# Kernel optimization log

Measured on AMD Instinct MI355X. Metric: run time of the kernel, lower is better.

## Reference

```python
import jax, jax.numpy as jnp
import numpy as np

B, S, D, H, NH, C = 32, 512, 768, 768, 4, 10
HD = H // NH


def _lin(x, w, b):
    return x @ w.T + b


def _ln(x, g, b, eps=1e-5):
    mu = jnp.mean(x, axis=-1, keepdims=True)
    var = jnp.mean(jnp.square(x - mu), axis=-1, keepdims=True)
    return (x - mu) * jax.lax.rsqrt(var + eps) * g + b


def setup_inputs() -> dict:
    key = jax.random.key(0)
    ks = jax.random.split(key, 16)
    w = lambda k, shape: jax.random.normal(k, shape, dtype=jnp.float32) * 0.02
    return {
        "x": jax.random.normal(ks[0], (B, S, D), dtype=jnp.float32),
        "wq": w(ks[1], (H, D)), "bq": jnp.zeros((H,), jnp.float32),
        "wk": w(ks[2], (H, D)), "bk": jnp.zeros((H,), jnp.float32),
        "wv": w(ks[3], (H, D)), "bv": jnp.zeros((H,), jnp.float32),
        "wx": w(ks[4], (H, D)), "bx": jnp.zeros((H,), jnp.float32),
        "in_proj_w": w(ks[5], (3 * H, H)), "in_proj_b": jnp.zeros((3 * H,), jnp.float32),
        "out_proj_w": w(ks[6], (H, H)), "out_proj_b": jnp.zeros((H,), jnp.float32),
        "fc1a_w": w(ks[7], (H, H)), "fc1a_b": jnp.zeros((H,), jnp.float32),
        "fc1b_w": w(ks[8], (H, H)), "fc1b_b": jnp.zeros((H,), jnp.float32),
        "ln_g": jnp.ones((H,), jnp.float32), "ln_b": jnp.zeros((H,), jnp.float32),
        "fc2_w": w(ks[9], (C, H)), "fc2_b": jnp.zeros((C,), jnp.float32),
    }


def reference(x, wq, bq, wk, bk, wv, bv, wx, bx, in_proj_w, in_proj_b,
              out_proj_w, out_proj_b, fc1a_w, fc1a_b, fc1b_w, fc1b_b,
              ln_g, ln_b, fc2_w, fc2_b):
    # Vectorized sinusoidal PE matching the triple loop:
    # even i: sin(pos / 10000^(2i/D)); odd i: cos(pos / 10000^(2(i-1)/D))
    d = x.shape[2]
    pos = jnp.arange(x.shape[1], dtype=x.dtype)[:, None]          # [S,1]
    i = jnp.arange(d)
    i_even = (i - (i % 2)).astype(x.dtype)                        # 2*(i - i%2)/d exponent
    angle = pos / jnp.power(jnp.asarray(10000.0, x.dtype), 2.0 * i_even / d)  # [S,D]
    pe = jnp.where(i % 2 == 0, jnp.sin(angle), jnp.cos(angle))
    x = x + pe[None]

    q = _lin(x, wq, bq)
    k = _lin(x, wk, bk)
    v = _lin(x, wv, bv)
    xr = _lin(x, wx, bx)

    # torch MultiheadAttention: in_proj, split heads, SDPA, out_proj
    wq_i, wk_i, wv_i = jnp.split(in_proj_w, 3, axis=0)
    bq_i, bk_i, bv_i = jnp.split(in_proj_b, 3, axis=0)
    b = x.shape[0]
    q2 = _lin(q, wq_i, bq_i).reshape(b, -1, NH, HD)
    k2 = _lin(k, wk_i, bk_i).reshape(b, -1, NH, HD)
    v2 = _lin(v, wv_i, bv_i).reshape(b, -1, NH, HD)
    scores = jnp.einsum('bqhd,bkhd->bhqk', q2, k2) / jnp.sqrt(jnp.asarray(HD, x.dtype))
    attn = jax.nn.softmax(scores, axis=-1)
    ctx = jnp.einsum('bhqk,bkhd->bqhd', attn, v2).reshape(b, -1, H)
    attn_out = _lin(ctx, out_proj_w, out_proj_b)

    x = _ln(xr + attn_out, ln_g, ln_b)
    ffn = _lin(jax.nn.relu(_lin(x, fc1a_w, fc1a_b)), fc1b_w, fc1b_b)
    x = _ln(x + ffn, ln_g, ln_b)
    x = jnp.sum(x, axis=1)
    return _lin(x, fc2_w, fc2_b)
```

## Files before the change

kernel.cpp:

```cpp
#include <hip/hip_runtime.h>
#include <hip/hip_bf16.h>

typedef __bf16 bf16;
typedef __bf16 bf16x8 __attribute__((ext_vector_type(8)));
typedef __bf16 bf16x4 __attribute__((ext_vector_type(4)));
typedef __bf16 bf16x2 __attribute__((ext_vector_type(2)));
typedef float  f32x4  __attribute__((ext_vector_type(4)));

#define GLD16(g, l) __builtin_amdgcn_global_load_lds(                        \
    (const __attribute__((address_space(1))) void*)(g),                      \
    (__attribute__((address_space(3))) void*)(l), 16, 0, 0)

template<int BM, int BN, int MFR, int NFR>
__global__ __launch_bounds__(256, 3)
void gemm_nt(const bf16* __restrict__ A, const bf16* __restrict__ B,
             bf16* __restrict__ C, const float* __restrict__ bias,
             int K, int lda, int ldb, int ldc,
             int inner,
             long long aOut, long long aIn,
             long long bOut, long long bIn,
             long long cOut, long long cIn,
             float alpha, int relu,
             const bf16* __restrict__ res, int ldr)
{
    const int z  = blockIdx.z;
    const int zo = z / inner;
    const int zi = z - zo * inner;
    A += (long long)zo * aOut + (long long)zi * aIn;
    B += (long long)zo * bOut + (long long)zi * bIn;
    C += (long long)zo * cOut + (long long)zi * cIn;

    const int tm = blockIdx.y * BM;
    const int tn = blockIdx.x * BN;

    __shared__ __align__(16) bf16 smem[(BM + BN) * 64];
    bf16* As = smem;
    bf16* Bs = smem + BM * 64;

    const int tid  = threadIdx.x;
    const int lane = tid & 63;
    const int wid  = tid >> 6;
    const int wr   = wid >> 1;
    const int wc   = wid & 1;

    f32x4 acc[MFR][NFR];
#pragma unroll
    for (int i = 0; i < MFR; ++i)
#pragma unroll
        for (int j = 0; j < NFR; ++j) acc[i][j] = (f32x4){0.f, 0.f, 0.f, 0.f};

    const int srow = lane >> 3;
    const int gch8 = ((lane & 7) ^ srow) * 8;

    const int NA = BM / 32;
    const int NB = BN / 32;

    const bf16* aP[NA];
#pragma unroll
    for (int jj = 0; jj < NA; ++jj) {
        const int R0 = (wid * NA + jj) * 8;
        aP[jj] = A + (long long)(tm + R0 + srow) * lda + gch8;
    }
    const bf16* bP[NB];
#pragma unroll
    for (int jj = 0; jj < NB; ++jj) {
        const int R0 = (wid * NB + jj) * 8;
        bP[jj] = B + (long long)(tn + R0 + srow) * ldb + gch8;
    }

    const int lr = lane & 15;
    const int qg = lane >> 4;

    for (int kt = 0; kt < K; kt += 64) {
#pragma unroll
        for (int jj = 0; jj < NA; ++jj)
            GLD16(aP[jj], As + (wid * NA + jj) * 512);
#pragma unroll
        for (int jj = 0; jj < NB; ++jj)
            GLD16(bP[jj], Bs + (wid * NB + jj) * 512);
        __syncthreads();

#pragma unroll
        for (int h = 0; h < 2; ++h) {
            const int off = ((qg + h * 4) ^ (lr & 7)) * 8;
            bf16x8 af[MFR], bfr[NFR];
#pragma unroll
            for (int i = 0; i < MFR; ++i)
                af[i] = *(const bf16x8*)(As + (wr * MFR * 16 + i * 16 + lr) * 64 + off);
#pragma unroll
            for (int j = 0; j < NFR; ++j)
                bfr[j] = *(const bf16x8*)(Bs + (wc * NFR * 16 + j * 16 + lr) * 64 + off);
#pragma unroll
            for (int i = 0; i < MFR; ++i)
#pragma unroll
                for (int j = 0; j < NFR; ++j)
                    acc[i][j] = __builtin_amdgcn_mfma_f32_16x16x32_bf16(
                        af[i], bfr[j], acc[i][j], 0, 0, 0);
        }
        __syncthreads();
#pragma unroll
        for (int jj = 0; jj < NA; ++jj) aP[jj] += 64;
#pragma unroll
        for (int jj = 0; jj < NB; ++jj) bP[jj] += 64;
    }

#pragma unroll
    for (int i = 0; i < MFR; ++i) {
#pragma unroll
        for (int j = 0; j < NFR; ++j) {
            const int mm0 = tm + wr * MFR * 16 + i * 16 + (lane >> 4) * 4;
            const int nn  = tn + wc * NFR * 16 + j * 16 + (lane & 15);
#pragma unroll
            for (int r = 0; r < 4; ++r) {
                float v = acc[i][j][r] * alpha;
                if (bias) v += bias[nn];
                if (res)  v += (float)res[(long long)(mm0 + r) * ldr + nn];
                if (relu) v = fmaxf(v, 0.f);
                C[(long long)(mm0 + r) * ldc + nn] = (bf16)v;
            }
        }
    }
}

#define BAR8()  __builtin_amdgcn_s_barrier()

#define RD_A(S, MB)                                                          \
    _Pragma("unroll") for (int mi = 0; mi < 4; ++mi)                         \
    _Pragma("unroll") for (int h = 0; h < 2; ++h)                            \
        af[mi][h] = *(const bf16x8*)((S) + aBase + ((MB) + mi) * 1024 +      \
                                     (h ? koff1 : koff0));

#define RD_B(S, NJ)                                                          \
    _Pragma("unroll") for (int h = 0; h < 2; ++h)                            \
        bfv[NJ][h] = *(const bf16x8*)((S) + bBase + (NJ) * 1024 +            \
                                      (h ? koff1 : koff0));

#define MFMA_Q(MB, N0, N1)                                                   \
    _Pragma("unroll") for (int h = 0; h < 2; ++h)                            \
    _Pragma("unroll") for (int mi = 0; mi < 4; ++mi) {                       \
        acc[(MB)+mi][(N0)] = __builtin_amdgcn_mfma_f32_16x16x32_bf16(        \
            af[mi][h], bfv[(N0)][h], acc[(MB)+mi][(N0)], 0, 0, 0);           \
        acc[(MB)+mi][(N1)] = __builtin_amdgcn_mfma_f32_16x16x32_bf16(        \
            af[mi][h], bfv[(N1)][h], acc[(MB)+mi][(N1)], 0, 0, 0);           \
    }

#define MFMA_Q1(MB, N0)                                                      \
    _Pragma("unroll") for (int h = 0; h < 2; ++h)                            \
    _Pragma("unroll") for (int mi = 0; mi < 4; ++mi) {                       \
        acc[(MB)+mi][(N0)] = __builtin_amdgcn_mfma_f32_16x16x32_bf16(        \
            af[mi][h], bfv[(N0)][h], acc[(MB)+mi][(N0)], 0, 0, 0);           \
    }

#define STAGE_A(DST)                                                         \
    _Pragma("unroll") for (int jj = 0; jj < 4; ++jj) {                       \
        GLD16(aP[jj], (DST) + (wid * 4 + jj) * 512);  aP[jj] += 64; }

#define STAGE_B(DST)                                                         \
    _Pragma("unroll") for (int jj = 0; jj < 4; ++jj) {                       \
        GLD16(bP[jj], (DST) + 16384 + (wid * 4 + jj) * 512);  bP[jj] += 64; }

#define STAGE_B3(DST)                                                        \
    _Pragma("unroll") for (int jj = 0; jj < 3; ++jj) {                       \
        GLD16(bP[jj], (DST) + 16384 + (wid * 3 + jj) * 512);  bP[jj] += 64; }

#define END_TILE()                                                           \
    asm volatile("s_waitcnt vmcnt(0)" ::: "memory");                         \
    __builtin_amdgcn_sched_barrier(0);                                       \
    BAR8();

#define K_TILE_F(CUR, NXT, STG, LAST)                                        \
  {                                                                          \
    RD_A((CUR), 0);                                                          \
    RD_B((CUR), 0); RD_B((CUR), 1); RD_B((CUR), 2); RD_B((CUR), 3);          \
    if (STG) { STAGE_A(NXT) STAGE_B(NXT) }                                   \
    MFMA_Q(0, 0, 1)                                                          \
    MFMA_Q(0, 2, 3)                                                          \
    RD_A((CUR), 4);                                                          \
    MFMA_Q(4, 2, 3)                                                          \
    MFMA_Q(4, 0, 1)                                                          \
    if (!(LAST)) { END_TILE() }                                              \
  }

#define K_TILE_F3(CUR, NXT, STG, LAST)                                       \
  {                                                                          \
    RD_A((CUR), 0);                                                          \
    RD_B((CUR), 0); RD_B((CUR), 1); RD_B((CUR), 2);                          \
    if (STG) { STAGE_A(NXT) STAGE_B3(NXT) }                                  \
    MFMA_Q(0, 0, 1)                                                          \
    MFMA_Q1(0, 2)                                                            \
    RD_A((CUR), 4);                                                          \
    MFMA_Q1(4, 2)                                                            \
    MFMA_Q(4, 0, 1)                                                          \
    if (!(LAST)) { END_TILE() }                                              \
  }

__global__ __launch_bounds__(512, 2)
void gemm_qkv_8ph(const bf16* __restrict__ A, const bf16* __restrict__ B,
                  bf16* __restrict__ C, const float* __restrict__ bias)
{
    constexpr int LDA = 768, LDB = 768, LDC = 3072;
    const int tm = blockIdx.y * 256;
    const int tn = blockIdx.x * 256;

    __shared__ __align__(16) bf16 smem[2][2 * 256 * 64];

    const int tid  = threadIdx.x;
    const int lane = tid & 63;
    const int wid  = tid >> 6;
    const int wr   = wid >> 2;
    const int wc   = wid & 3;
    const int lr   = lane & 15;
    const int qg   = lane >> 4;

    const int srow = lane >> 3;
    const int gch8 = ((lane & 7) ^ srow) * 8;
    const bf16* aP[4];
    const bf16* bP[4];
#pragma unroll
    for (int jj = 0; jj < 4; ++jj) {
        aP[jj] = A + (long long)(tm + wid * 32 + jj * 8 + srow) * LDA + gch8;
        bP[jj] = B + (long long)(tn + wid * 32 + jj * 8 + srow) * LDB + gch8;
    }

    f32x4 acc[8][4];
#pragma unroll
    for (int i = 0; i < 8; ++i)
#pragma unroll
        for (int j = 0; j < 4; ++j) acc[i][j] = (f32x4){0.f, 0.f, 0.f, 0.f};

    const int aBase = (wr * 128 + lr) * 64;
    const int bBase = 16384 + (wc * 64 + lr) * 64;
    const int koff0 = ((qg    ) ^ (lr & 7)) * 8;
    const int koff1 = ((qg + 4) ^ (lr & 7)) * 8;

    bf16x8 af[4][2];
    bf16x8 bfv[4][2];

    bf16* S0 = &smem[0][0];
    bf16* S1 = &smem[1][0];

    STAGE_A(S0)
    STAGE_B(S0)
    asm volatile("s_waitcnt vmcnt(0)" ::: "memory");
    __builtin_amdgcn_sched_barrier(0);
    BAR8();

#pragma unroll 1
    for (int it = 0; it < 5; ++it) {
        K_TILE_F(S0, S1, 1, 0)
        K_TILE_F(S1, S0, 1, 0)
    }
    K_TILE_F(S0, S1, 1, 0)
    K_TILE_F(S1, S0, 0, 1)

    float bv[4];
#pragma unroll
    for (int j = 0; j < 4; ++j) bv[j] = bias[tn + wc * 64 + j * 16 + lr];

#pragma unroll
    for (int i = 0; i < 8; ++i) {
        const int mm0 = tm + wr * 128 + i * 16 + qg * 4;
#pragma unroll
        for (int j = 0; j < 4; ++j) {
            const int nn = tn + wc * 64 + j * 16 + lr;
#pragma unroll
            for (int r = 0; r < 4; ++r)
                C[(long long)(mm0 + r) * LDC + nn] = (bf16)(acc[i][j][r] + bv[j]);
        }
    }
}

__global__ __launch_bounds__(512, 2)
void gemm_flow(const bf16* __restrict__ A, const bf16* __restrict__ B,
               bf16* __restrict__ C, const float* __restrict__ bias,
               int lda, int ldb, int ldc, int relu,
               const bf16* __restrict__ res, int ldr)
{
    const int tm = blockIdx.y * 256;
    const int tn = blockIdx.x * 192;

    __shared__ __align__(16) bf16 smem[2][(256 + 192) * 64];

    const int tid  = threadIdx.x;
    const int lane = tid & 63;
    const int wid  = tid >> 6;
    const int wr   = wid >> 2;
    const int wc   = wid & 3;
    const int lr   = lane & 15;
    const int qg   = lane >> 4;

    const int srow = lane >> 3;
    const int gch8 = ((lane & 7) ^ srow) * 8;
    const bf16* aP[4];
    const bf16* bP[3];
#pragma unroll
    for (int jj = 0; jj < 4; ++jj)
        aP[jj] = A + (long long)(tm + wid * 32 + jj * 8 + srow) * lda + gch8;
#pragma unroll
    for (int jj = 0; jj < 3; ++jj)
        bP[jj] = B + (long long)(tn + wid * 24 + jj * 8 + srow) * ldb + gch8;

    f32x4 acc[8][3];
#pragma unroll
    for (int i = 0; i < 8; ++i)
#pragma unroll
        for (int j = 0; j < 3; ++j) acc[i][j] = (f32x4){0.f, 0.f, 0.f, 0.f};

    const int aBase = (wr * 128 + lr) * 64;
    const int bBase = 16384 + (wc * 48 + lr) * 64;
    const int koff0 = ((qg    ) ^ (lr & 7)) * 8;
    const int koff1 = ((qg + 4) ^ (lr & 7)) * 8;

    bf16x8 af[4][2];
    bf16x8 bfv[3][2];

    bf16* S0 = &smem[0][0];
    bf16* S1 = &smem[1][0];

    STAGE_A(S0)
    STAGE_B3(S0)
    asm volatile("s_waitcnt vmcnt(0)" ::: "memory");
    __builtin_amdgcn_sched_barrier(0);
    BAR8();

#pragma unroll 1
    for (int it = 0; it < 5; ++it) {
        K_TILE_F3(S0, S1, 1, 0)
        K_TILE_F3(S1, S0, 1, 0)
    }
    K_TILE_F3(S0, S1, 1, 0)
    K_TILE_F3(S1, S0, 0, 1)

    float bv[3];
#pragma unroll
    for (int j = 0; j < 3; ++j) bv[j] = bias ? bias[tn + wc * 48 + j * 16 + lr] : 0.f;

#pragma unroll
    for (int i = 0; i < 8; ++i) {
        const int mm0 = tm + wr * 128 + i * 16 + qg * 4;
#pragma unroll
        for (int j = 0; j < 3; ++j) {
            const int nn = tn + wc * 48 + j * 16 + lr;
#pragma unroll
            for (int r = 0; r < 4; ++r) {
                float v = acc[i][j][r] + bv[j];
                if (res)  v += (float)res[(long long)(mm0 + r) * ldr + nn];
                if (relu) v = fmaxf(v, 0.f);
                C[(long long)(mm0 + r) * ldc + nn] = (bf16)v;
            }
        }
    }
}

__global__ __launch_bounds__(256, 2)
void fused_attn_kernel(bf16* __restrict__ qkvx)
{
    const int flat = blockIdx.x;
    const int qt = (flat >> 3) & 3;
    const int z  = (flat & 7) | ((flat >> 5) << 3);
    const int b  = z >> 2, h = z & 3;

    const bf16* Qg = qkvx + (long long)b * 512 * 3072 + h * 192;
    const bf16* Kg = Qg + 768;
    const bf16* Vg = Qg + 1536;

    __shared__ __align__(16) bf16 Ks[64 * 192];
    __shared__ __align__(16) bf16 VTs[192 * 64];
    __shared__ __align__(16) bf16 Pb[4 * 32 * 64];

    const int tid  = threadIdx.x;
    const int lane = tid & 63;
    const int wid  = tid >> 6;
    const int lr   = lane & 15;
    const int qg   = lane >> 4;
    const int m0   = qt * 128 + wid * 32;

    bf16x8 qf[2][6];
#pragma unroll
    for (int mt = 0; mt < 2; ++mt)
#pragma unroll
        for (int t = 0; t < 6; ++t)
            qf[mt][t] = *(const bf16x8*)(Qg + (long long)(m0 + mt * 16 + lr) * 3072
                                         + t * 32 + qg * 8);

    const bf16* kP[6];
#pragma unroll
    for (int i = 0; i < 6; ++i) {
        const int c = i * 256 + tid;
        const int krow = c / 24, kcc = c % 24;
        const int kgc  = (kcc & 24) | ((kcc & 7) ^ (krow & 7));
        kP[i] = Kg + (long long)krow * 3072 + kgc * 8;
    }
    const int vkp = tid & 31;
    const int vdc = tid >> 5;

    f32x4 acc[2][12];
#pragma unroll
    for (int mt = 0; mt < 2; ++mt)
#pragma unroll
        for (int dt = 0; dt < 12; ++dt) acc[mt][dt] = (f32x4){0.f, 0.f, 0.f, 0.f};
    float mrow[2][4], lrow[2][4];
#pragma unroll
    for (int mt = 0; mt < 2; ++mt)
#pragma unroll
        for (int r = 0; r < 4; ++r) { mrow[mt][r] = -3e38f; lrow[mt][r] = 0.f; }

    const float alpha = 0.0721687836f;

    for (int kt = 0; kt < 8; ++kt) {
#pragma unroll
        for (int i = 0; i < 6; ++i)
            GLD16(kP[i], Ks + (i * 256 + wid * 64) * 8);
#pragma unroll
        for (int i = 0; i < 3; ++i) {
            const int dc = vdc + i * 8;
            const bf16* p = Vg + (long long)(2 * vkp) * 3072 + dc * 8;
            const bf16x8 v0 = *(const bf16x8*)(p);
            const bf16x8 v1 = *(const bf16x8*)(p + 3072);
#pragma unroll
            for (int j = 0; j < 8; ++j) {
                const int d = dc * 8 + j;
                bf16x2 pk; pk[0] = v0[j]; pk[1] = v1[j];
                *(bf16x2*)(VTs + d * 64 + ((vkp >> 2) ^ (d & 7)) * 8
                           + 2 * (vkp & 3)) = pk;
            }
        }
        __syncthreads();

        f32x4 sf[2][4];
#pragma unroll
        for (int mt = 0; mt < 2; ++mt)
#pragma unroll
            for (int nt = 0; nt < 4; ++nt) sf[mt][nt] = (f32x4){0.f, 0.f, 0.f, 0.f};
#pragma unroll
        for (int nt = 0; nt < 4; ++nt) {
#pragma unroll
            for (int t = 0; t < 6; ++t) {
                const int ch = t * 4 + qg;
                const int ph = (ch & 24) | ((ch & 7) ^ (lr & 7));
                const bf16x8 kf = *(const bf16x8*)(Ks + (nt * 16 + lr) * 192 + ph * 8);
                sf[0][nt] = __builtin_amdgcn_mfma_f32_16x16x32_bf16(qf[0][t], kf, sf[0][nt], 0, 0, 0);
                sf[1][nt] = __builtin_amdgcn_mfma_f32_16x16x32_bf16(qf[1][t], kf, sf[1][nt], 0, 0, 0);
            }
        }

#pragma unroll
        for (int mt = 0; mt < 2; ++mt) {
            float mx[4], a[4], rs[4], p[4][4];
#pragma unroll
            for (int r = 0; r < 4; ++r) {
                float v0 = fmaxf(sf[mt][0][r], sf[mt][1][r]);
                float v1 = fmaxf(sf[mt][2][r], sf[mt][3][r]);
                mx[r] = fmaxf(v0, v1) * alpha;
            }
#pragma unroll
            for (int msk = 1; msk <= 8; msk <<= 1)
#pragma unroll
                for (int r = 0; r < 4; ++r) mx[r] = fmaxf(mx[r], __shfl_xor(mx[r], msk));
#pragma unroll
            for (int r = 0; r < 4; ++r) {
                const float mn = fmaxf(mrow[mt][r], mx[r]);
                a[r] = __expf(mrow[mt][r] - mn);
                mrow[mt][r] = mn;
                rs[r] = 0.f;
            }
#pragma unroll
            for (int nt = 0; nt < 4; ++nt)
#pragma unroll
                for (int r = 0; r < 4; ++r) {
                    p[nt][r] = __expf(sf[mt][nt][r] * alpha - mrow[mt][r]);
                    rs[r] += p[nt][r];
                }
#pragma unroll
            for (int msk = 1; msk <= 8; msk <<= 1)
#pragma unroll
                for (int r = 0; r < 4; ++r) rs[r] += __shfl_xor(rs[r], msk);
#pragma unroll
            for (int r = 0; r < 4; ++r) lrow[mt][r] = lrow[mt][r] * a[r] + rs[r];
#pragma unroll
            for (int dt = 0; dt < 12; ++dt)
#pragma unroll
                for (int r = 0; r < 4; ++r) acc[mt][dt][r] *= a[r];
#pragma unroll
            for (int nt = 0; nt < 4; ++nt)
#pragma unroll
                for (int r = 0; r < 4; ++r) {
                    const int row = mt * 16 + qg * 4 + r;
                    const int ph2 = (nt * 2 + (lr >> 3)) ^ (row & 7);
                    Pb[wid * 2048 + row * 64 + ph2 * 8 + (lr & 7)] = (bf16)p[nt][r];
                }
        }

        bf16x8 pf[2][2];
#pragma unroll
        for (int mt = 0; mt < 2; ++mt)
#pragma unroll
            for (int ks = 0; ks < 2; ++ks) {
                const int row = mt * 16 + lr;
                const int ph  = (ks * 4 + qg) ^ (lr & 7);
                pf[mt][ks] = *(const bf16x8*)(Pb + wid * 2048 + row * 64 + ph * 8);
            }
#pragma unroll
        for (int dt = 0; dt < 12; ++dt) {
#pragma unroll
            for (int ks = 0; ks < 2; ++ks) {
                const int ph = (ks * 4 + qg) ^ (lr & 7);
                const bf16x8 vf = *(const bf16x8*)(VTs + (dt * 16 + lr) * 64 + ph * 8);
                acc[0][dt] = __builtin_amdgcn_mfma_f32_16x16x32_bf16(pf[0][ks], vf, acc[0][dt], 0, 0, 0);
                acc[1][dt] = __builtin_amdgcn_mfma_f32_16x16x32_bf16(pf[1][ks], vf, acc[1][dt], 0, 0, 0);
            }
        }
        __syncthreads();
#pragma unroll
        for (int i = 0; i < 6; ++i) kP[i] += 64 * 3072;
        Vg += 64 * 3072;
    }

    bf16* Og = qkvx + (long long)b * 512 * 3072 + h * 192;
#pragma unroll
    for (int mt = 0; mt < 2; ++mt) {
        float inv[4];
#pragma unroll
        for (int r = 0; r < 4; ++r) inv[r] = 1.0f / lrow[mt][r];
#pragma unroll
        for (int dt = 0; dt < 12; ++dt)
#pragma unroll
            for (int r = 0; r < 4; ++r) {
                const int row = m0 + mt * 16 + qg * 4 + r;
                Og[(long long)row * 3072 + dt * 16 + lr] = (bf16)(acc[mt][dt][r] * inv[r]);
            }
    }
}

__device__ __forceinline__ void cast4(const float* src, bf16* dst, int i)
{
    const float4 v = *(const float4*)(src + (long long)i * 4);
    bf16x4 o;
    o[0] = (bf16)v.x; o[1] = (bf16)v.y; o[2] = (bf16)v.z; o[3] = (bf16)v.w;
    *(bf16x4*)(dst + (long long)i * 4) = o;
}

__global__ __launch_bounds__(256)
void prep_kernel(const float* __restrict__ wq, const float* __restrict__ wk,
                 const float* __restrict__ wv, const float* __restrict__ wx,
                 const float* __restrict__ inpw, const float* __restrict__ inpb,
                 const float* __restrict__ bq, const float* __restrict__ bk,
                 const float* __restrict__ bv, const float* __restrict__ bx,
                 const float* __restrict__ woutp, const float* __restrict__ wf1a,
                 const float* __restrict__ wf1b, const float* __restrict__ x,
                 bf16* __restrict__ WT3, bf16* __restrict__ INPJ,
                 bf16* __restrict__ WOUT, bf16* __restrict__ WF1A,
                 bf16* __restrict__ WF1B, bf16* __restrict__ WXD,
                 float* __restrict__ BCAT, bf16* __restrict__ XPE)
{
    const int blk = blockIdx.x;
    const int tid = threadIdx.x;
    __shared__ bf16 t[32][33];

    if (blk < 1728) {
        const int which = blk / 576, local = blk - which * 576;
        const float* src = (which == 0) ? wq : ((which == 1) ? wk : wv);
        bf16* dst = WT3 + (long long)which * 589824;
        const int r0 = (local / 24) * 32, c0 = (local % 24) * 32;
        const int tr = tid >> 5, tc = tid & 31;
#pragma unroll
        for (int k = 0; k < 4; ++k) {
            const int r = tr + k * 8;
            t[r][tc] = (bf16)src[(long long)(r0 + r) * 768 + c0 + tc];
        }
        __syncthreads();
#pragma unroll
        for (int k = 0; k < 4; ++k) {
            const int c = tr + k * 8;
            dst[(long long)(c0 + c) * 768 + r0 + tc] = t[tc][c];
        }
    } else if (blk < 3456) {
        cast4(inpw, INPJ, (blk - 1728) * 256 + tid);
    } else if (blk < 4032) {
        cast4(woutp, WOUT, (blk - 3456) * 256 + tid);
    } else if (blk < 4608) {
        cast4(wf1a, WF1A, (blk - 4032) * 256 + tid);
    } else if (blk < 5184) {
        cast4(wf1b, WF1B, (blk - 4608) * 256 + tid);
    } else if (blk < 5760) {
        cast4(wx, WXD, (blk - 5184) * 256 + tid);
    } else if (blk < 6051) {
        const int bl = blk - 5760;
        if (bl < 288) {
            const int g = tid >> 5, l = tid & 31;
            const int n = bl * 8 + g;
            const int zsec = n / 768;
            const float* bb = (zsec == 0) ? bq : ((zsec == 1) ? bk : bv);
            const float* wrow = inpw + (long long)n * 768;
            float s = 0.f;
            for (int d = l; d < 768; d += 32) s += wrow[d] * bb[d];
#pragma unroll
            for (int off = 16; off; off >>= 1) s += __shfl_xor(s, off);
            if (l == 0) BCAT[n] = inpb[n] + s;
        } else {
            const int n = (bl - 288) * 256 + tid;
            if (n < 768) BCAT[2304 + n] = bx[n];
        }
    } else {
        const int idx4 = ((blk - 6051) * 256 + tid) * 4;
        const int d    = idx4 % 768;
        const int row  = idx4 / 768;
        const int s    = row & 511;
        const float ksc = -0.034603417655076f;
        const float4 xv = *(const float4*)(x + (long long)idx4);
        float a0 = (float)s * exp2f((float)d * ksc);
        float a1 = (float)s * exp2f((float)(d + 2) * ksc);
        float s0, c0, s1, c1;
        sincosf(a0, &s0, &c0);
        sincosf(a1, &s1, &c1);
        bf16x4 o;
        o[0] = (bf16)(xv.x + s0);
        o[1] = (bf16)(xv.y + c0);
        o[2] = (bf16)(xv.z + s1);
        o[3] = (bf16)(xv.w + c1);
        *(bf16x4*)(XPE + (long long)idx4) = o;
    }
}

__global__ __launch_bounds__(256)
void ln1_kernel(const bf16* __restrict__ a, int lda_,
                bf16* __restrict__ o, int ldo,
                const float* __restrict__ g, const float* __restrict__ be)
{
    const int blk  = blockIdx.x;
    const int tid  = threadIdx.x;
    const int wid  = tid >> 6, lane = tid & 63;
    const int d0   = lane * 12;

    float gv[12], ev[12];
#pragma unroll
    for (int k = 0; k < 12; k += 4) {
        *(float4*)(gv + k) = *(const float4*)(g + d0 + k);
        *(float4*)(ev + k) = *(const float4*)(be + d0 + k);
    }

    for (int i = 0; i < 8; ++i) {
        const int row = blk * 32 + i * 4 + wid;
        const bf16* p = a + (long long)row * lda_ + d0;
        float xv[12];
#pragma unroll
        for (int k = 0; k < 12; k += 4) {
            const bf16x4 v = *(const bf16x4*)(p + k);
            xv[k] = (float)v[0]; xv[k+1] = (float)v[1];
            xv[k+2] = (float)v[2]; xv[k+3] = (float)v[3];
        }
        float s1 = 0.f, s2 = 0.f;
#pragma unroll
        for (int k = 0; k < 12; ++k) { s1 += xv[k]; s2 += xv[k] * xv[k]; }
        for (int off = 32; off; off >>= 1) {
            s1 += __shfl_xor(s1, off);
            s2 += __shfl_xor(s2, off);
        }
        const float mu  = s1 * (1.0f / 768.0f);
        const float var = s2 * (1.0f / 768.0f) - mu * mu;
        const float rs  = rsqrtf(var + 1e-5f);
        bf16* po = o + (long long)row * ldo + d0;
#pragma unroll
        for (int k = 0; k < 12; k += 4) {
            bf16x4 ov;
            ov[0] = (bf16)((xv[k]   - mu) * rs * gv[k]   + ev[k]);
            ov[1] = (bf16)((xv[k+1] - mu) * rs * gv[k+1] + ev[k+1]);
            ov[2] = (bf16)((xv[k+2] - mu) * rs * gv[k+2] + ev[k+2]);
            ov[3] = (bf16)((xv[k+3] - mu) * rs * gv[k+3] + ev[k+3]);
            *(bf16x4*)(po + k) = ov;
        }
    }
}

__global__ __launch_bounds__(256)
void ln2_reduce_kernel(const bf16* __restrict__ src,
                       const float* __restrict__ g, const float* __restrict__ be,
                       float* __restrict__ partial)
{
    const int blk  = blockIdx.x;
    const int tid  = threadIdx.x;
    const int wid  = tid >> 6, lane = tid & 63;
    const int d0   = lane * 12;

    float gv[12], ev[12];
#pragma unroll
    for (int k = 0; k < 12; k += 4) {
        *(float4*)(gv + k) = *(const float4*)(g + d0 + k);
        *(float4*)(ev + k) = *(const float4*)(be + d0 + k);
    }
    float acc[12];
#pragma unroll
    for (int k = 0; k < 12; ++k) acc[k] = 0.f;

    for (int i = 0; i < 8; ++i) {
        const int row = blk * 32 + i * 4 + wid;
        const bf16* p = src + (long long)row * 3072 + d0;
        float xv[12];
#pragma unroll
        for (int k = 0; k < 12; k += 4) {
            const bf16x4 v = *(const bf16x4*)(p + k);
            xv[k] = (float)v[0]; xv[k+1] = (float)v[1];
            xv[k+2] = (float)v[2]; xv[k+3] = (float)v[3];
        }
        float s1 = 0.f, s2 = 0.f;
#pragma unroll
        for (int k = 0; k < 12; ++k) { s1 += xv[k]; s2 += xv[k] * xv[k]; }
        for (int off = 32; off; off >>= 1) {
            s1 += __shfl_xor(s1, off);
            s2 += __shfl_xor(s2, off);
        }
        const float mu  = s1 * (1.0f / 768.0f);
        const float var = s2 * (1.0f / 768.0f) - mu * mu;
        const float rs  = rsqrtf(var + 1e-5f);
#pragma unroll
        for (int k = 0; k < 12; ++k) acc[k] += (xv[k] - mu) * rs * gv[k] + ev[k];
    }

    __shared__ float red[4][768];
#pragma unroll
    for (int k = 0; k < 12; k += 4)
        *(float4*)(&red[wid][d0 + k]) = *(const float4*)(acc + k);
    __syncthreads();
    if (wid == 0) {
#pragma unroll
        for (int k = 0; k < 12; k += 4) {
            const float4 a0 = *(const float4*)(&red[0][d0 + k]);
            const float4 a1 = *(const float4*)(&red[1][d0 + k]);
            const float4 a2 = *(const float4*)(&red[2][d0 + k]);
            const float4 a3 = *(const float4*)(&red[3][d0 + k]);
            *(float4*)(partial + (long long)blk * 768 + d0 + k) =
                make_float4(a0.x + a1.x + a2.x + a3.x, a0.y + a1.y + a2.y + a3.y,
                            a0.z + a1.z + a2.z + a3.z, a0.w + a1.w + a2.w + a3.w);
        }
    }
}

__global__ __launch_bounds__(192)
void reduce_fc2_stage2_kernel(const float* __restrict__ partial, const float* __restrict__ w,
                              const float* __restrict__ bias, float* __restrict__ out)
{
    const int b = blockIdx.x, t = threadIdx.x;
    const int d0 = t * 4;
    float a[4] = {0.f, 0.f, 0.f, 0.f};
    for (int c = 0; c < 16; ++c) {
        const float4 pv = *(const float4*)(partial + (long long)(b * 16 + c) * 768 + d0);
        a[0] += pv.x; a[1] += pv.y; a[2] += pv.z; a[3] += pv.w;
    }
    __shared__ float os[10];
    if (t < 10) os[t] = 0.f;
    __syncthreads();
    for (int c = 0; c < 10; ++c) {
        const float4 wv = *(const float4*)(w + c * 768 + d0);
        float p = wv.x * a[0] + wv.y * a[1] + wv.z * a[2] + wv.w * a[3];
        for (int off = 32; off; off >>= 1) p += __shfl_xor(p, off);
        if ((t & 63) == 0) atomicAdd(&os[c], p);
    }
    __syncthreads();
    if (t < 10) out[b * 10 + t] = os[t] + bias[t];
}

static const size_t OFF_XPE  = 0;
static const size_t OFF_WCAT = OFF_XPE  + (size_t)16384 * 768 * 2;
static const size_t OFF_WT3  = OFF_WCAT + (size_t)3072 * 768 * 2;
static const size_t OFF_INPJ = OFF_WT3  + (size_t)3 * 768 * 768 * 2;
static const size_t OFF_WOUT = OFF_INPJ + (size_t)2304 * 768 * 2;
static const size_t OFF_WF1A = OFF_WOUT + (size_t)768 * 768 * 2;
static const size_t OFF_WF1B = OFF_WF1A + (size_t)768 * 768 * 2;
static const size_t OFF_BCAT = OFF_WF1B + (size_t)768 * 768 * 2;
static const size_t OFF_QKVX = OFF_BCAT + (size_t)3072 * 4;
static const size_t OFF_VT   = OFF_QKVX + (size_t)16384 * 3072 * 2;
static const size_t OFF_S    = OFF_VT   + (size_t)128 * 192 * 512 * 2;
static const size_t OFF_X1   = OFF_S    + (size_t)128 * 512 * 512 * 2;

extern "C" void kernel_launch(void* const* d_in, const int* in_sizes, int n_in,
                              void* d_out, int out_size, void* d_ws, size_t ws_size,
                              hipStream_t stream)
{
    const float* x     = (const float*)d_in[0];
    const float* wq    = (const float*)d_in[1];
    const float* bq    = (const float*)d_in[2];
    const float* wk    = (const float*)d_in[3];
    const float* bk    = (const float*)d_in[4];
    const float* wv    = (const float*)d_in[5];
    const float* bv    = (const float*)d_in[6];
    const float* wx    = (const float*)d_in[7];
    const float* bx    = (const float*)d_in[8];
    const float* inpw  = (const float*)d_in[9];
    const float* inpb  = (const float*)d_in[10];
    const float* woutp = (const float*)d_in[11];
    const float* boutp = (const float*)d_in[12];
    const float* wf1a  = (const float*)d_in[13];
    const float* bf1a  = (const float*)d_in[14];
    const float* wf1b  = (const float*)d_in[15];
    const float* bf1b  = (const float*)d_in[16];
    const float* lng   = (const float*)d_in[17];
    const float* lnb   = (const float*)d_in[18];
    const float* wfc2  = (const float*)d_in[19];
    const float* bfc2  = (const float*)d_in[20];
    float* out = (float*)d_out;

    char* ws = (char*)d_ws;
    bf16*  XPE  = (bf16*)(ws + OFF_XPE);
    bf16*  WCAT = (bf16*)(ws + OFF_WCAT);
    bf16*  WT3  = (bf16*)(ws + OFF_WT3);
    bf16*  INPJ = (bf16*)(ws + OFF_INPJ);
    bf16*  WOUT = (bf16*)(ws + OFF_WOUT);
    bf16*  WF1A = (bf16*)(ws + OFF_WF1A);
    bf16*  WF1B = (bf16*)(ws + OFF_WF1B);
    float* BCAT = (float*)(ws + OFF_BCAT);
    bf16*  QKVX = (bf16*)(ws + OFF_QKVX);
    float* PART = (float*)(ws + OFF_S);
    bf16*  X1   = (bf16*)(ws + OFF_X1);

    prep_kernel<<<18339, 256, 0, stream>>>(wq, wk, wv, wx, inpw, inpb,
                                           bq, bk, bv, bx, woutp, wf1a, wf1b, x,
                                           WT3, INPJ, WOUT, WF1A, WF1B,
                                           WCAT + (size_t)2304 * 768, BCAT, XPE);

    gemm_nt<64, 128, 2, 4><<<dim3(6, 12, 3), 256, 0, stream>>>(
        INPJ, WT3, WCAT, nullptr, 768, 768, 768, 768,
        1, 589824, 0, 589824, 0, 589824, 0, 1.0f, 0, nullptr, 0);

    gemm_qkv_8ph<<<dim3(12, 64, 1), 512, 0, stream>>>(XPE, WCAT, QKVX, BCAT);

    fused_attn_kernel<<<512, 256, 0, stream>>>(QKVX);

    gemm_flow<<<dim3(4, 64, 1), 512, 0, stream>>>(
        QKVX, WOUT, QKVX + 768, boutp, 3072, 768, 3072,
        0, QKVX + 2304, 3072);

    ln1_kernel<<<512, 256, 0, stream>>>(QKVX + 768, 3072, X1, 768, lng, lnb);

    gemm_flow<<<dim3(4, 64, 1), 512, 0, stream>>>(
        X1, WF1A, QKVX + 1536, bf1a, 768, 768, 3072,
        1, nullptr, 0);

    gemm_flow<<<dim3(4, 64, 1), 512, 0, stream>>>(
        QKVX + 1536, WF1B, QKVX + 2304, bf1b, 3072, 768, 3072,
        0, X1, 768);

    ln2_reduce_kernel<<<512, 256, 0, stream>>>(QKVX + 2304, lng, lnb, PART);

    reduce_fc2_stage2_kernel<<<32, 192, 0, stream>>>(PART, wfc2, bfc2, out);
}
```

Before: 443.7 us.

## Restructure QKV GEMM K-loop into phased in-place staging with wave priority

The QKV projection GEMM's main loop now preloads two K tiles and refills each shared-memory buffer in place as soon as its sub-tiles have been read, instead of staging the next tile at the start. Loads are interleaved between four MFMA phases separated by workgroup barriers, and the wait is relaxed to vmcnt(4) so one tile's loads stay in flight. MFMA phases run under raised wave priority via s_setprio. The aim is to overlap global-to-LDS traffic with compute and drop the full vmcnt(0) stall each tile, at the cost of extra barriers per tile and tighter correctness dependencies on barrier placement.

```diff
diff --git a/kernel.cpp b/kernel.cpp
--- a/kernel.cpp
+++ b/kernel.cpp
@@ -144,6 +144,11 @@
             af[mi][h], bfv[(N1)][h], acc[(MB)+mi][(N1)], 0, 0, 0);           \
     }
 
+#define MFMA_QP(MB, N0, N1)                                                  \
+    __builtin_amdgcn_s_setprio(1);                                           \
+    MFMA_Q(MB, N0, N1)                                                       \
+    __builtin_amdgcn_s_setprio(0);
+
 #define MFMA_Q1(MB, N0)                                                      \
     _Pragma("unroll") for (int h = 0; h < 2; ++h)                            \
     _Pragma("unroll") for (int mi = 0; mi < 4; ++mi) {                       \
@@ -155,10 +160,6 @@
     _Pragma("unroll") for (int jj = 0; jj < 4; ++jj) {                       \
         GLD16(aP[jj], (DST) + (wid * 4 + jj) * 512);  aP[jj] += 64; }
 
-#define STAGE_B(DST)                                                         \
-    _Pragma("unroll") for (int jj = 0; jj < 4; ++jj) {                       \
-        GLD16(bP[jj], (DST) + 16384 + (wid * 4 + jj) * 512);  bP[jj] += 64; }
-
 #define STAGE_B3(DST)                                                        \
     _Pragma("unroll") for (int jj = 0; jj < 3; ++jj) {                       \
         GLD16(bP[jj], (DST) + 16384 + (wid * 3 + jj) * 512);  bP[jj] += 64; }
@@ -167,19 +168,6 @@
     asm volatile("s_waitcnt vmcnt(0)" ::: "memory");                         \
     __builtin_amdgcn_sched_barrier(0);                                       \
     BAR8();
-
-#define K_TILE_F(CUR, NXT, STG, LAST)                                        \
-  {                                                                          \
-    RD_A((CUR), 0);                                                          \
-    RD_B((CUR), 0); RD_B((CUR), 1); RD_B((CUR), 2); RD_B((CUR), 3);          \
-    if (STG) { STAGE_A(NXT) STAGE_B(NXT) }                                   \
-    MFMA_Q(0, 0, 1)                                                          \
-    MFMA_Q(0, 2, 3)                                                          \
-    RD_A((CUR), 4);                                                          \
-    MFMA_Q(4, 2, 3)                                                          \
-    MFMA_Q(4, 0, 1)                                                          \
-    if (!(LAST)) { END_TILE() }                                              \
-  }
 
 #define K_TILE_F3(CUR, NXT, STG, LAST)                                       \
   {                                                                          \
@@ -194,6 +182,33 @@
     if (!(LAST)) { END_TILE() }                                              \
   }
 
+#define SUA(q, DST) { GLD16(aU[q], (DST) + (q) * 4096 + tid * 8);  aU[q] += 64; }
+#define SUB(q, DST) { GLD16(bU[q], (DST) + 16384 + (q) * 4096 + tid * 8);  bU[q] += 64; }
+
+#define GATE_V4() asm volatile("s_waitcnt vmcnt(4)" ::: "memory");           \
+                  __builtin_amdgcn_sched_barrier(0); BAR8();
+#define GATE_V0() asm volatile("s_waitcnt vmcnt(0)" ::: "memory");           \
+                  __builtin_amdgcn_sched_barrier(0); BAR8();
+
+#define K_TILE_M(S, STG, GMODE)                                              \
+  {                                                                          \
+    RD_A((S), 0); RD_B((S), 0); RD_B((S), 1);                                \
+    MFMA_QP(0, 0, 1)                                                         \
+    BAR8();                                                                  \
+    RD_B((S), 2); RD_B((S), 3);                                              \
+    if (STG) { SUA(0, (S)) SUA(2, (S)) }                                     \
+    MFMA_QP(0, 2, 3)                                                         \
+    BAR8();                                                                  \
+    RD_A((S), 4);                                                            \
+    if (STG) { SUB(0, (S)) SUB(1, (S)) SUB(2, (S)) }                         \
+    MFMA_QP(4, 2, 3)                                                         \
+    BAR8();                                                                  \
+    if (STG) { SUB(3, (S)) SUA(1, (S)) SUA(3, (S)) }                         \
+    MFMA_QP(4, 0, 1)                                                         \
+    if ((GMODE) == 1) { GATE_V4() }                                          \
+    if ((GMODE) == 2) { GATE_V0() }                                          \
+  }
+
 __global__ __launch_bounds__(512, 2)
 void gemm_qkv_8ph(const bf16* __restrict__ A, const bf16* __restrict__ B,
                   bf16* __restrict__ C, const float* __restrict__ bias)
@@ -212,14 +227,14 @@
     const int lr   = lane & 15;
     const int qg   = lane >> 4;
 
-    const int srow = lane >> 3;
-    const int gch8 = ((lane & 7) ^ srow) * 8;
-    const bf16* aP[4];
-    const bf16* bP[4];
-#pragma unroll
-    for (int jj = 0; jj < 4; ++jj) {
-        aP[jj] = A + (long long)(tm + wid * 32 + jj * 8 + srow) * LDA + gch8;
-        bP[jj] = B + (long long)(tn + wid * 32 + jj * 8 + srow) * LDB + gch8;
+    const int urow = tid >> 3;
+    const int uch  = ((tid & 7) ^ (urow & 7)) * 8;
+    const bf16* aU[4];
+    const bf16* bU[4];
+#pragma unroll
+    for (int q = 0; q < 4; ++q) {
+        aU[q] = A + (long long)(tm + q * 64 + urow) * LDA + uch;
+        bU[q] = B + (long long)(tn + q * 64 + urow) * LDB + uch;
     }
 
     f32x4 acc[8][4];
@@ -239,19 +254,23 @@
     bf16* S0 = &smem[0][0];
     bf16* S1 = &smem[1][0];
 
-    STAGE_A(S0)
-    STAGE_B(S0)
-    asm volatile("s_waitcnt vmcnt(0)" ::: "memory");
-    __builtin_amdgcn_sched_barrier(0);
-    BAR8();
+#pragma unroll
+    for (int q = 0; q < 4; ++q) SUA(q, S0)
+#pragma unroll
+    for (int q = 0; q < 4; ++q) SUB(q, S0)
+#pragma unroll
+    for (int q = 0; q < 4; ++q) SUA(q, S1)
+#pragma unroll
+    for (int q = 0; q < 4; ++q) SUB(q, S1)
+    GATE_V4()
 
 #pragma unroll 1
     for (int it = 0; it < 5; ++it) {
-        K_TILE_F(S0, S1, 1, 0)
-        K_TILE_F(S1, S0, 1, 0)
-    }
-    K_TILE_F(S0, S1, 1, 0)
-    K_TILE_F(S1, S0, 0, 1)
+        K_TILE_M(S0, 1, 1)
+        K_TILE_M(S1, 1, 1)
+    }
+    K_TILE_M(S0, 0, 2)
+    K_TILE_M(S1, 0, 0)
 
     float bv[4];
 #pragma unroll
```

After: 458.6 us. +3.4%, slower.
